# Kernel optimization log

Measured on AMD Instinct MI355X. Metric: run time of the kernel, lower is better.

Reference implementation:

```python
import jax, jax.numpy as jnp
import numpy as np

E, N, C, A, S, H, HD, RH = 320000, 20000, 128, 4, 16, 8, 32, 64
AH = H * HD  # 256 attn-head channels; mul_alpha = AH, mul_alpha_head = HD
OUT = 128


def smooth_leaky_relu(x, a=0.2):
    # Equiformer SmoothLeakyReLU: 0.5*((1+a)*x + (1-a)*x*(2*sigmoid(x)-1))
    return 0.5 * ((1 + a) * x + (1 - a) * x * (2.0 * jax.nn.sigmoid(x) - 1.0))


def setup_inputs() -> dict:
    key = jax.random.key(0)
    ks = jax.random.split(key, 20)
    d = {
        'message': jax.random.normal(ks[0], (E, C), jnp.float32),
        'edge_attr': jax.random.normal(ks[1], (E, A), jnp.float32),
        'edge_scalars': jax.random.normal(ks[2], (E, S), jnp.float32),
        'w_rad1': jax.random.normal(ks[3], (S, RH), jnp.float32) / np.sqrt(S),
        'b_rad1': jnp.zeros((RH,), jnp.float32),
        'w_rad2': jax.random.normal(ks[4], (RH, C * A), jnp.float32) / np.sqrt(RH),
        'b_rad2': jnp.zeros((C * A,), jnp.float32),
        'w_dtp_v': jax.random.normal(ks[5], (C, A), jnp.float32) / np.sqrt(A),
        'w_lin_act': jax.random.normal(ks[6], (C, C), jnp.float32) / np.sqrt(C),
        'b_lin_act': jnp.zeros((C,), jnp.float32),
        'w_alpha': jax.random.normal(ks[7], (C, AH), jnp.float32) / np.sqrt(C),
        'b_alpha': jnp.zeros((AH,), jnp.float32),
        'w_lin_v': jax.random.normal(ks[8], (C, AH), jnp.float32) / np.sqrt(C),
        'b_lin_v': jnp.zeros((AH,), jnp.float32),
        'alpha_dot': jax.random.normal(ks[9], (H, HD), jnp.float32) / np.sqrt(HD),
        'w_proj': jax.random.normal(ks[10], (AH, OUT), jnp.float32) / np.sqrt(AH),
        'b_proj': jnp.zeros((OUT,), jnp.float32),
        'edge_dst': jax.random.randint(ks[11], (E,), 0, N, jnp.int32),
        'n_nodes_dst': N,
    }
    return d


def reference(message, edge_attr, edge_scalars,
              w_rad1, b_rad1, w_rad2, b_rad2,
              w_dtp_v, w_lin_act, b_lin_act,
              w_alpha, b_alpha, w_lin_v, b_lin_v,
              alpha_dot, w_proj, b_proj,
              edge_dst, n_nodes_dst):
    n = n_nodes_dst
    # dtp_rad: radial MLP -> per-edge depthwise TP weights [E, C, A]
    h = jax.nn.silu(edge_scalars @ w_rad1 + b_rad1)
    w = (h @ w_rad2 + b_rad2).reshape(-1, C, A)
    # sep_act.dtp (scalar irreps): out[e,c] = msg[e,c] * sum_a w[e,c,a]*attr[e,a]
    msg = message * jnp.einsum('eca,ea->ec', w, edge_attr)
    # sep_alpha -> alpha heads [E, H, HD]
    alpha = (msg @ w_alpha + b_alpha).reshape(-1, H, HD)
    # sep_act.lin + gate (scalars -> SiLU)
    value = jax.nn.silu(msg @ w_lin_act + b_lin_act)
    # sep_value: internal-weight dtp then linear, reshape to heads
    value = value * jnp.einsum('ca,ea->ec', w_dtp_v, edge_attr)
    value = (value @ w_lin_v + b_lin_v).reshape(-1, H, HD)
    # attention logits
    alpha = smooth_leaky_relu(alpha)
    alpha = jnp.einsum('ehk,hk->eh', alpha, alpha_dot)
    # scatter softmax over destination nodes
    amax = jax.ops.segment_max(alpha, edge_dst, num_segments=n)  # [N, H]
    amax = jnp.where(jnp.isfinite(amax), amax, 0.0)
    ex = jnp.exp(alpha - amax[edge_dst])
    denom = jax.ops.segment_sum(ex, edge_dst, num_segments=n)
    alpha = ex / (denom[edge_dst] + 1e-16)
    # weighted scatter-add aggregation
    attn = value * alpha[..., None]  # [E, H, HD]
    node = jax.ops.segment_sum(attn, edge_dst, num_segments=n)  # [N, H, HD]
    node = node.reshape(n, AH)  # heads2vec
    return node @ w_proj + b_proj
```

## Files before the change

### kernel.cpp

```cpp
#include <hip/hip_runtime.h>
#include <hip/hip_bf16.h>

#define C_   128
#define A_   4
#define S_   16
#define RH_  64
#define H_   8
#define AH_  256
#define OUT_ 128

typedef __attribute__((ext_vector_type(8))) short bf16x8;
typedef __attribute__((ext_vector_type(4))) float f32x4;

__device__ __forceinline__ float sigf(float x) { return 1.0f / (1.0f + __expf(-x)); }

__device__ __forceinline__ unsigned short f2bf(float x) {
    unsigned u = __float_as_uint(x);
    unsigned r = (u + 0x7fffu + ((u >> 16) & 1u)) >> 16;
    return (unsigned short)r;
}
__device__ __forceinline__ float bf2f(unsigned short v) {
    return __uint_as_float((unsigned)v << 16);
}

__device__ __forceinline__ unsigned pkbf(float a, float b) {
    union { __hip_bfloat162 h; unsigned u; } c;
    c.h = __float22bfloat162_rn(float2{a, b});
    return c.u;
}

__device__ __forceinline__ unsigned enc(float x) {
    unsigned b = __float_as_uint(x);
    return (b & 0x80000000u) ? ~b : (b | 0x80000000u);
}
__device__ __forceinline__ float dec(unsigned u) {
    unsigned b = (u & 0x80000000u) ? (u & 0x7fffffffu) : ~u;
    return __uint_as_float(b);
}

__global__ void k_pack(const float* __restrict__ W, short* __restrict__ out, int K, int N) {
    const int KS = K / 32;
    const int ct = blockIdx.x / KS, ks = blockIdx.x % KS;
    const int l = threadIdx.x, lr = l & 15, lg = l >> 4;
    bf16x8 v;
    #pragma unroll
    for (int j = 0; j < 8; j++)
        v[j] = (short)f2bf(W[(size_t)(ks * 32 + lg * 8 + j) * N + ct * 16 + lr]);
    *(bf16x8*)&out[((size_t)blockIdx.x * 64 + l) * 8] = v;
}

__global__ void k_pack_dtp(const float* __restrict__ W, short* __restrict__ out) {
    const int ct = blockIdx.x >> 3, ks = blockIdx.x & 7;
    const int l = threadIdx.x, lr = l & 15, lg = l >> 4;
    bf16x8 v;
    #pragma unroll
    for (int j = 0; j < 8; j++)
        v[j] = (short)f2bf(W[(size_t)(ks * 8 + lg * 2 + (j >> 2)) * 512 + (ct * 16 + lr) * 4 + (j & 3)]);
    *(bf16x8*)&out[((size_t)blockIdx.x * 64 + l) * 8] = v;
}

__global__ __launch_bounds__(256) void k_hist(
    const int* __restrict__ edge_dst, int* __restrict__ deg, int E)
{
    const int e = blockIdx.x * 256 + threadIdx.x;
    if (e < E) atomicAdd(&deg[edge_dst[e]], 1);
}

__global__ __launch_bounds__(1024) void k_scan(
    const int* __restrict__ deg, int* __restrict__ cursor, int N)
{
    __shared__ int part[1024];
    const int t = threadIdx.x;
    const int per = (N + 1023) / 1024;
    const int i0 = t * per;
    int s = 0;
    for (int i = 0; i < per; i++) { int idx = i0 + i; if (idx < N) s += deg[idx]; }
    part[t] = s;
    __syncthreads();
    for (int off = 1; off < 1024; off <<= 1) {
        int v = (t >= off) ? part[t - off] : 0;
        __syncthreads();
        part[t] += v;
        __syncthreads();
    }
    int excl = (t == 0) ? 0 : part[t - 1];
    for (int i = 0; i < per; i++) {
        int idx = i0 + i;
        if (idx < N) { cursor[idx] = excl; excl += deg[idx]; }
    }
}

__global__ __launch_bounds__(256) void k_fill(
    const int* __restrict__ edge_dst, int* __restrict__ cursor,
    int* __restrict__ sorted, int E)
{
    const int e = blockIdx.x * 256 + threadIdx.x;
    if (e < E) {
        const int pos = atomicAdd(&cursor[edge_dst[e]], 1);
        sorted[pos] = e;
    }
}

__global__ __launch_bounds__(256, 4) void k_msgalpha(
    const float* __restrict__ message, const float* __restrict__ edge_attr,
    const float* __restrict__ edge_scalars,
    const float* __restrict__ w_rad1, const float* __restrict__ b_rad1,
    const short* __restrict__ w_rad2_lin, const float* __restrict__ b_rad2,
    const short* __restrict__ w_alpha_lin, const float* __restrict__ b_alpha,
    const float* __restrict__ alpha_dot, const int* __restrict__ edge_dst,
    short* __restrict__ msg_bf, float* __restrict__ logits, unsigned* __restrict__ amax_u)
{
    __shared__ __align__(16) char smem[25216];
    short* Ap     = (short*)smem;
    short* msg_s  = (short*)(smem + 16384);
    float* w1_s   = (float*)(smem + 16384);
    float* es_s   = (float*)(smem + 16384 + 4096);
    float* attr_s = (float*)(smem + 24576);
    int*   dst_s  = (int*)(smem + 25088);

    const int t = threadIdx.x;
    const long e0 = (long)blockIdx.x * 32;

    *(float4*)&w1_s[t * 4] = *(const float4*)&w_rad1[t * 4];
    if (t < 128) {
        const int r = t >> 2, s4 = (t & 3) * 4;
        *(float4*)&es_s[r * 17 + s4] = *(const float4*)&edge_scalars[(e0 + r) * S_ + s4];
    }
    if (t < 32) {
        *(float4*)&attr_s[t * 4] = *(const float4*)&edge_attr[(e0 + t) * A_];
        dst_s[t] = edge_dst[e0 + t];
    }
    __syncthreads();

    {
        const int r = t & 31, o0 = (t >> 5) * 8;
        float acc[8];
        #pragma unroll
        for (int i = 0; i < 8; i++) acc[i] = b_rad1[o0 + i];
        #pragma unroll
        for (int s = 0; s < S_; s++) {
            const float ev = es_s[r * 17 + s];
            #pragma unroll
            for (int i = 0; i < 8; i++) acc[i] += ev * w1_s[s * 64 + o0 + i];
        }
        float h[8];
        #pragma unroll
        for (int i = 0; i < 8; i++) { const float x = acc[i]; h[i] = x * sigf(x); }
        const float4 a4 = *(const float4*)&attr_s[r * 4];
        char* base = (char*)Ap + r * 512;
        const int sw = (r & 31) << 4;
        #pragma unroll
        for (int c = 0; c < 4; c++) {
            const float h0 = h[2 * c], h1 = h[2 * c + 1];
            uint4 v;
            v.x = pkbf(h0 * a4.x, h0 * a4.y);
            v.y = pkbf(h0 * a4.z, h0 * a4.w);
            v.z = pkbf(h1 * a4.x, h1 * a4.y);
            v.w = pkbf(h1 * a4.z, h1 * a4.w);
            *(uint4*)(base + ((o0 * 8 + c * 16) ^ sw)) = v;
        }
    }
    __syncthreads();

    const int w = t >> 6, l = t & 63, lr = l & 15, lg = l >> 4;

    {
        #pragma unroll
        for (int q = 0; q < 2; q++) {
            const int ct = w * 2 + q;
            bf16x8 bf[8];
            #pragma unroll
            for (int ks = 0; ks < 8; ks++)
                bf[ks] = *(const bf16x8*)&w_rad2_lin[((size_t)(ct * 8 + ks) * 64 + l) * 8];
            const int col = ct * 16 + lr;
            const float4 b2 = *(const float4*)&b_rad2[col * 4];
            #pragma unroll
            for (int rt = 0; rt < 2; rt++) {
                const int arow = rt * 16 + lr;
                const char* abase = (char*)Ap + arow * 512;
                const int asw = (arow & 31) << 4;
                bf16x8 af[8];
                #pragma unroll
                for (int ks = 0; ks < 8; ks++)
                    af[ks] = *(const bf16x8*)(abase + ((ks * 64 + lg * 16) ^ asw));
                f32x4 acc = {0.f, 0.f, 0.f, 0.f};
                #pragma unroll
                for (int ks = 0; ks < 8; ks++)
                    acc = __builtin_amdgcn_mfma_f32_16x16x32_bf16(af[ks], bf[ks], acc, 0, 0, 0);
                #pragma unroll
                for (int r = 0; r < 4; r++) {
                    const int row = rt * 16 + lg * 4 + r;
                    const float4 a4 = *(const float4*)&attr_s[row * 4];
                    const float badj = a4.x * b2.x + a4.y * b2.y + a4.z * b2.z + a4.w * b2.w;
                    const float m = message[(e0 + row) * C_ + col];
                    *(short*)((char*)msg_s + row * 256 + ((col * 2) ^ ((row & 15) << 4))) =
                        (short)f2bf(m * (acc[r] + badj));
                }
            }
        }
    }
    __syncthreads();

    {
        #pragma unroll
        for (int i = 0; i < 2; i++) {
            const int q = t + i * 256;
            const int row = q >> 4, ch = q & 15;
            const uint4 v = *(const uint4*)((char*)msg_s + row * 256 + ((ch * 16) ^ ((row & 15) << 4)));
            *(uint4*)((char*)msg_bf + ((e0 + row) * 256 + ch * 16)) = v;
        }
    }

    {
        #pragma unroll
        for (int hq = 0; hq < 2; hq++) {
            const int hd = w * 2 + hq;
            bf16x8 waf[2][4];
            float4 ba4[2], ad4[2];
            #pragma unroll
            for (int q = 0; q < 2; q++) {
                const int ctw = hd * 2 + q;
                #pragma unroll
                for (int ks = 0; ks < 4; ks++)
                    waf[q][ks] = *(const bf16x8*)&w_alpha_lin[((size_t)(ctw * 4 + ks) * 64 + l) * 8];
                ba4[q] = *(const float4*)&b_alpha[ctw * 16 + lg * 4];
                ad4[q] = *(const float4*)&alpha_dot[ctw * 16 + lg * 4];
            }
            #pragma unroll
            for (int ct = 0; ct < 2; ct++) {
                const int erow = ct * 16 + lr;
                const char* mbase = (char*)msg_s + erow * 256;
                const int msw = (erow & 15) << 4;
                bf16x8 mb[4];
                #pragma unroll
                for (int ks = 0; ks < 4; ks++)
                    mb[ks] = *(const bf16x8*)(mbase + ((ks * 64 + lg * 16) ^ msw));
                float s = 0.f;
                #pragma unroll
                for (int q = 0; q < 2; q++) {
                    f32x4 acc = {0.f, 0.f, 0.f, 0.f};
                    #pragma unroll
                    for (int ks = 0; ks < 4; ks++)
                        acc = __builtin_amdgcn_mfma_f32_16x16x32_bf16(waf[q][ks], mb[ks], acc, 0, 0, 0);
                    #pragma unroll
                    for (int r = 0; r < 4; r++) {
                        const float x = acc[r] + ((const float*)&ba4[q])[r];
                        const float y = x * (0.2f + 0.8f * sigf(x));
                        s += y * ((const float*)&ad4[q])[r];
                    }
                }
                s += __shfl_xor(s, 16);
                s += __shfl_xor(s, 32);
                if (lg == 0) {
                    const long e = e0 + ct * 16 + lr;
                    logits[e * H_ + hd] = s;
                    atomicMax(&amax_u[dst_s[ct * 16 + lr] * H_ + hd], enc(s));
                }
            }
        }
    }
}

__global__ __launch_bounds__(256) void k_denom(
    const float* __restrict__ logits, const int* __restrict__ edge_dst,
    const unsigned* __restrict__ amax_u, float* __restrict__ denom, int EH)
{
    const int t = blockIdx.x * 256 + threadIdx.x;
    if (t >= EH) return;
    const int e = t >> 3, h = t & 7;
    const int n = edge_dst[e];
    const float am = dec(amax_u[n * H_ + h]);
    atomicAdd(&denom[n * H_ + h], __expf(logits[t] - am));
}

__global__ __launch_bounds__(256, 5) void k_value(
    const short* __restrict__ msg_bf, const float* __restrict__ edge_attr,
    const short* __restrict__ w_lin_act_lin, const float* __restrict__ b_lin_act,
    const float* __restrict__ w_dtp_v,
    const short* __restrict__ w_lin_v_lin, const float* __restrict__ b_lin_v,
    const float* __restrict__ logits, const int* __restrict__ edge_dst,
    const unsigned* __restrict__ amax_u, const float* __restrict__ denom,
    const int* __restrict__ sorted, float* __restrict__ node)
{
    __shared__ __align__(16) char pool[16896];
    __shared__ float attr_s[32][4];
    __shared__ float wgt_s[32][H_];
    __shared__ int   dst_s[32];
    __shared__ int   eid_s[32];
    short* a_s  = (short*)pool;
    short* v_s  = (short*)(pool + 8192);
    short* val2 = (short*)pool;

    const int t = threadIdx.x;
    const int b0 = blockIdx.x * 32;

    if (t < 32) {
        const int e = sorted[b0 + t];
        eid_s[t] = e;
        dst_s[t] = edge_dst[e];
        *(float4*)&attr_s[t][0] = *(const float4*)&edge_attr[(long)e * A_];
    }
    __syncthreads();
    #pragma unroll
    for (int i = 0; i < 2; i++) {
        const int q = t + i * 256;
        const int row = q >> 4, ch = q & 15;
        const uint4 v = *(const uint4*)((const char*)msg_bf + ((long)eid_s[row] * 256 + ch * 16));
        *(uint4*)((char*)a_s + row * 256 + ((ch * 16) ^ ((row & 15) << 4))) = v;
    }
    {
        const int el = t >> 3, h = t & 7;
        const long e = eid_s[el];
        const int n = dst_s[el];
        const float am = dec(amax_u[n * H_ + h]);
        const float d  = denom[n * H_ + h];
        wgt_s[el][h] = __expf(logits[e * H_ + h] - am) / (d + 1e-16f);
    }
    __syncthreads();

    const int w = t >> 6, l = t & 63, lr = l & 15, lg = l >> 4;
    {
        bf16x8 af[2][4];
        #pragma unroll
        for (int rt = 0; rt < 2; rt++)
            #pragma unroll
            for (int ks = 0; ks < 4; ks++) {
                const int arow = rt * 16 + lr;
                af[rt][ks] = *(bf16x8*)((char*)a_s + arow * 256 + ((ks * 64 + lg * 16) ^ ((arow & 15) << 4)));
            }
        #pragma unroll
        for (int q = 0; q < 2; q++) {
            const int ct = w * 2 + q;
            bf16x8 bfg[4];
            #pragma unroll
            for (int ks = 0; ks < 4; ks++)
                bfg[ks] = *(const bf16x8*)&w_lin_act_lin[((size_t)(ct * 4 + ks) * 64 + l) * 8];
            const int col = ct * 16 + lr;
            const float bb = b_lin_act[col];
            const float4 wv = *(const float4*)&w_dtp_v[col * 4];
            #pragma unroll
            for (int rt = 0; rt < 2; rt++) {
                f32x4 acc = {0.f, 0.f, 0.f, 0.f};
                #pragma unroll
                for (int ks = 0; ks < 4; ks++)
                    acc = __builtin_amdgcn_mfma_f32_16x16x32_bf16(af[rt][ks], bfg[ks], acc, 0, 0, 0);
                #pragma unroll
                for (int r = 0; r < 4; r++) {
                    const int row = rt * 16 + lg * 4 + r;
                    float x = acc[r] + bb;
                    x = x * sigf(x);
                    const float4 a4 = *(const float4*)&attr_s[row][0];
                    const float dv = wv.x * a4.x + wv.y * a4.y + wv.z * a4.z + wv.w * a4.w;
                    *(short*)((char*)v_s + row * 256 + ((col * 2) ^ ((row & 15) << 4))) =
                        (short)f2bf(x * dv);
                }
            }
        }
    }
    __syncthreads();

    bf16x8 vf[2][4];
    #pragma unroll
    for (int rt = 0; rt < 2; rt++)
        #pragma unroll
        for (int ks = 0; ks < 4; ks++) {
            const int row = rt * 16 + lr;
            vf[rt][ks] = *(bf16x8*)((char*)v_s + row * 256 + ((ks * 64 + lg * 16) ^ ((row & 15) << 4)));
        }
    __syncthreads();

    #pragma unroll
    for (int q = 0; q < 4; q++) {
        const int ct = w * 4 + q;
        bf16x8 bf[4];
        #pragma unroll
        for (int ks = 0; ks < 4; ks++)
            bf[ks] = *(const bf16x8*)&w_lin_v_lin[((size_t)(ct * 4 + ks) * 64 + l) * 8];
        const int col = ct * 16 + lr;
        const float bb = b_lin_v[col];
        #pragma unroll
        for (int rt = 0; rt < 2; rt++) {
            f32x4 acc = {0.f, 0.f, 0.f, 0.f};
            #pragma unroll
            for (int ks = 0; ks < 4; ks++)
                acc = __builtin_amdgcn_mfma_f32_16x16x32_bf16(vf[rt][ks], bf[ks], acc, 0, 0, 0);
            #pragma unroll
            for (int r = 0; r < 4; r++) {
                const int row = rt * 16 + lg * 4 + r;
                val2[row * 264 + col] = (short)f2bf((acc[r] + bb) * wgt_s[row][col >> 5]);
            }
        }
    }
    __syncthreads();
    {
        const int c = t;
        float run = 0.f;
        int s = 0;
        #pragma unroll 1
        for (int e = 0; e < 32; e++) {
            run += bf2f((unsigned short)val2[e * 264 + c]);
            const bool end = (e == 31) || (dst_s[e + 1] != dst_s[e]);
            if (end) {
                float* np = node + (long)dst_s[e] * AH_ + c;
                if (s == 0 || e == 31) atomicAdd(np, run);
                else *np = run;
                run = 0.f; s = e + 1;
            }
        }
    }
}

__global__ __launch_bounds__(256) void k_proj(
    const float* __restrict__ node, const float* __restrict__ w_proj,
    const float* __restrict__ b_proj, float* __restrict__ out)
{
    __shared__ float node_s[32][AH_];
    const int t = threadIdx.x;
    const long n0 = (long)blockIdx.x * 32;
    #pragma unroll
    for (int i = 0; i < 8; i++) {
        const int idx = t + i * 256;
        const int nl = idx >> 6, c4 = (idx & 63) * 4;
        *(float4*)&node_s[nl][c4] = *(const float4*)&node[(n0 + nl) * AH_ + c4];
    }
    __syncthreads();
    const int j0 = (t & 31) * 4;
    const int g  = t >> 5;
    float4 acc4[4];
    const float4 b = *(const float4*)&b_proj[j0];
    #pragma unroll
    for (int i = 0; i < 4; i++) acc4[i] = b;
    const float* wp = w_proj + j0;
    for (int c4 = 0; c4 < 64; c4++) {
        const float4 w0 = *(const float4*)&wp[(c4 * 4 + 0) * OUT_];
        const float4 w1 = *(const float4*)&wp[(c4 * 4 + 1) * OUT_];
        const float4 w2 = *(const float4*)&wp[(c4 * 4 + 2) * OUT_];
        const float4 w3 = *(const float4*)&wp[(c4 * 4 + 3) * OUT_];
        #pragma unroll
        for (int i = 0; i < 4; i++) {
            const float4 nv = *(const float4*)&node_s[g * 4 + i][c4 * 4];
            acc4[i].x += nv.x * w0.x + nv.y * w1.x + nv.z * w2.x + nv.w * w3.x;
            acc4[i].y += nv.x * w0.y + nv.y * w1.y + nv.z * w2.y + nv.w * w3.y;
            acc4[i].z += nv.x * w0.z + nv.y * w1.z + nv.z * w2.z + nv.w * w3.z;
            acc4[i].w += nv.x * w0.w + nv.y * w1.w + nv.z * w2.w + nv.w * w3.w;
        }
    }
    #pragma unroll
    for (int i = 0; i < 4; i++) {
        const long n = n0 + g * 4 + i;
        *(float4*)&out[n * OUT_ + j0] = acc4[i];
    }
}

extern "C" void kernel_launch(void* const* d_in, const int* in_sizes, int n_in,
                              void* d_out, int out_size, void* d_ws, size_t ws_size,
                              hipStream_t stream)
{
    const float* message      = (const float*)d_in[0];
    const float* edge_attr    = (const float*)d_in[1];
    const float* edge_scalars = (const float*)d_in[2];
    const float* w_rad1       = (const float*)d_in[3];
    const float* b_rad1       = (const float*)d_in[4];
    const float* w_rad2       = (const float*)d_in[5];
    const float* b_rad2       = (const float*)d_in[6];
    const float* w_dtp_v      = (const float*)d_in[7];
    const float* w_lin_act    = (const float*)d_in[8];
    const float* b_lin_act    = (const float*)d_in[9];
    const float* w_alpha      = (const float*)d_in[10];
    const float* b_alpha      = (const float*)d_in[11];
    const float* w_lin_v      = (const float*)d_in[12];
    const float* b_lin_v      = (const float*)d_in[13];
    const float* alpha_dot    = (const float*)d_in[14];
    const float* w_proj       = (const float*)d_in[15];
    const float* b_proj       = (const float*)d_in[16];
    const int*   edge_dst     = (const int*)d_in[17];

    const int E = in_sizes[0] / C_;
    const int N = out_size / OUT_;

    char* ws = (char*)d_ws;
    float*    node     = (float*)ws;
    unsigned* amax_u   = (unsigned*)(node + (size_t)N * AH_);
    float*    denom    = (float*)(amax_u + (size_t)N * H_);
    int*      deg      = (int*)(denom + (size_t)N * H_);
    int*      cursor   = deg + N;
    int*      sorted   = cursor + N;
    short*    w_rad2_l = (short*)(sorted + E);
    short*    w_alph_l = w_rad2_l + 64 * 512;
    short*    w_lact_l = w_alph_l + 128 * 256;
    short*    w_linv_l = w_lact_l + 128 * 128;
    short*    msg_bf   = w_linv_l + 128 * 256;
    float*    logits   = (float*)(msg_bf + (size_t)E * C_);

    hipMemsetAsync(d_ws, 0, (size_t)N * (AH_ + 2 * H_ + 1) * 4, stream);

    const int nbE256 = (E + 255) / 256;
    k_pack_dtp<<<64, 64, 0, stream>>>(w_rad2, w_rad2_l);
    k_pack<<<(256/16)*(128/32), 64, 0, stream>>>(w_alpha,   w_alph_l, 128, 256);
    k_pack<<<(128/16)*(128/32), 64, 0, stream>>>(w_lin_act, w_lact_l, 128, 128);
    k_pack<<<(256/16)*(128/32), 64, 0, stream>>>(w_lin_v,   w_linv_l, 128, 256);
    k_hist<<<nbE256, 256, 0, stream>>>(edge_dst, deg, E);
    k_scan<<<1, 1024, 0, stream>>>(deg, cursor, N);
    k_fill<<<nbE256, 256, 0, stream>>>(edge_dst, cursor, sorted, E);
    k_msgalpha<<<E / 32, 256, 0, stream>>>(message, edge_attr, edge_scalars,
                                           w_rad1, b_rad1, w_rad2_l, b_rad2,
                                           w_alph_l, b_alpha, alpha_dot, edge_dst,
                                           msg_bf, logits, amax_u);
    k_denom<<<(E * H_ + 255) / 256, 256, 0, stream>>>(logits, edge_dst, amax_u, denom, E * H_);
    k_value<<<E / 32, 256, 0, stream>>>(msg_bf, edge_attr, w_lact_l, b_lin_act, w_dtp_v,
                                        w_linv_l, b_lin_v, logits, edge_dst, amax_u, denom,
                                        sorted, node);
    k_proj<<<N / 32, 256, 0, stream>>>(node, w_proj, b_proj, (float*)d_out);
}
```

Before: 407.2 us.

## Cut register pressure in msgalpha and aggregate softmax denominators over sorted edges

```diff
diff --git a/kernel.cpp b/kernel.cpp
--- a/kernel.cpp
+++ b/kernel.cpp
@@ -101,7 +101,7 @@
     }
 }
 
-__global__ __launch_bounds__(256, 4) void k_msgalpha(
+__global__ __launch_bounds__(256, 5) void k_msgalpha(
     const float* __restrict__ message, const float* __restrict__ edge_attr,
     const float* __restrict__ edge_scalars,
     const float* __restrict__ w_rad1, const float* __restrict__ b_rad1,
@@ -168,10 +168,6 @@
         #pragma unroll
         for (int q = 0; q < 2; q++) {
             const int ct = w * 2 + q;
-            bf16x8 bf[8];
-            #pragma unroll
-            for (int ks = 0; ks < 8; ks++)
-                bf[ks] = *(const bf16x8*)&w_rad2_lin[((size_t)(ct * 8 + ks) * 64 + l) * 8];
             const int col = ct * 16 + lr;
             const float4 b2 = *(const float4*)&b_rad2[col * 4];
             #pragma unroll
@@ -179,14 +175,19 @@
                 const int arow = rt * 16 + lr;
                 const char* abase = (char*)Ap + arow * 512;
                 const int asw = (arow & 31) << 4;
-                bf16x8 af[8];
-                #pragma unroll
-                for (int ks = 0; ks < 8; ks++)
-                    af[ks] = *(const bf16x8*)(abase + ((ks * 64 + lg * 16) ^ asw));
                 f32x4 acc = {0.f, 0.f, 0.f, 0.f};
                 #pragma unroll
-                for (int ks = 0; ks < 8; ks++)
-                    acc = __builtin_amdgcn_mfma_f32_16x16x32_bf16(af[ks], bf[ks], acc, 0, 0, 0);
+                for (int kc = 0; kc < 2; kc++) {
+                    bf16x8 bf[4], af[4];
+                    #pragma unroll
+                    for (int ks = 0; ks < 4; ks++) {
+                        bf[ks] = *(const bf16x8*)&w_rad2_lin[((size_t)(ct * 8 + kc * 4 + ks) * 64 + l) * 8];
+                        af[ks] = *(const bf16x8*)(abase + (((kc * 4 + ks) * 64 + lg * 16) ^ asw));
+                    }
+                    #pragma unroll
+                    for (int ks = 0; ks < 4; ks++)
+                        acc = __builtin_amdgcn_mfma_f32_16x16x32_bf16(af[ks], bf[ks], acc, 0, 0, 0);
+                }
                 #pragma unroll
                 for (int r = 0; r < 4; r++) {
                     const int row = rt * 16 + lg * 4 + r;
@@ -215,46 +216,46 @@
         #pragma unroll
         for (int hq = 0; hq < 2; hq++) {
             const int hd = w * 2 + hq;
-            bf16x8 waf[2][4];
-            float4 ba4[2], ad4[2];
+            float s0 = 0.f, s1 = 0.f;
             #pragma unroll
             for (int q = 0; q < 2; q++) {
                 const int ctw = hd * 2 + q;
+                bf16x8 waf[4];
                 #pragma unroll
                 for (int ks = 0; ks < 4; ks++)
-                    waf[q][ks] = *(const bf16x8*)&w_alpha_lin[((size_t)(ctw * 4 + ks) * 64 + l) * 8];
-                ba4[q] = *(const float4*)&b_alpha[ctw * 16 + lg * 4];
-                ad4[q] = *(const float4*)&alpha_dot[ctw * 16 + lg * 4];
-            }
-            #pragma unroll
-            for (int ct = 0; ct < 2; ct++) {
-                const int erow = ct * 16 + lr;
-                const char* mbase = (char*)msg_s + erow * 256;
-                const int msw = (erow & 15) << 4;
-                bf16x8 mb[4];
+                    waf[ks] = *(const bf16x8*)&w_alpha_lin[((size_t)(ctw * 4 + ks) * 64 + l) * 8];
+                const float4 ba4 = *(const float4*)&b_alpha[ctw * 16 + lg * 4];
+                const float4 ad4 = *(const float4*)&alpha_dot[ctw * 16 + lg * 4];
                 #pragma unroll
-                for (int ks = 0; ks < 4; ks++)
-                    mb[ks] = *(const bf16x8*)(mbase + ((ks * 64 + lg * 16) ^ msw));
-                float s = 0.f;
-                #pragma unroll
-                for (int q = 0; q < 2; q++) {
+                for (int ct = 0; ct < 2; ct++) {
+                    const int erow = ct * 16 + lr;
+                    const char* mbase = (char*)msg_s + erow * 256;
+                    const int msw = (erow & 15) << 4;
                     f32x4 acc = {0.f, 0.f, 0.f, 0.f};
                     #pragma unroll
-                    for (int ks = 0; ks < 4; ks++)
-                        acc = __builtin_amdgcn_mfma_f32_16x16x32_bf16(waf[q][ks], mb[ks], acc, 0, 0, 0);
+                    for (int ks = 0; ks < 4; ks++) {
+                        const bf16x8 mb = *(const bf16x8*)(mbase + ((ks * 64 + lg * 16) ^ msw));
+                        acc = __builtin_amdgcn_mfma_f32_16x16x32_bf16(waf[ks], mb, acc, 0, 0, 0);
+                    }
+                    float sl = 0.f;
                     #pragma unroll
                     for (int r = 0; r < 4; r++) {
-                        const float x = acc[r] + ((const float*)&ba4[q])[r];
+                        const float x = acc[r] + ((const float*)&ba4)[r];
                         const float y = x * (0.2f + 0.8f * sigf(x));
-                        s += y * ((const float*)&ad4[q])[r];
+                        sl += y * ((const float*)&ad4)[r];
                     }
+                    if (ct == 0) s0 += sl; else s1 += sl;
                 }
-                s += __shfl_xor(s, 16);
-                s += __shfl_xor(s, 32);
+            }
+            #pragma unroll
+            for (int ct = 0; ct < 2; ct++) {
+                float v = (ct == 0) ? s0 : s1;
+                v += __shfl_xor(v, 16);
+                v += __shfl_xor(v, 32);
                 if (lg == 0) {
                     const long e = e0 + ct * 16 + lr;
-                    logits[e * H_ + hd] = s;
-                    atomicMax(&amax_u[dst_s[ct * 16 + lr] * H_ + hd], enc(s));
+                    logits[e * H_ + hd] = v;
+                    atomicMax(&amax_u[dst_s[ct * 16 + lr] * H_ + hd], enc(v));
                 }
             }
         }
@@ -263,14 +264,25 @@
 
 __global__ __launch_bounds__(256) void k_denom(
     const float* __restrict__ logits, const int* __restrict__ edge_dst,
-    const unsigned* __restrict__ amax_u, float* __restrict__ denom, int EH)
-{
-    const int t = blockIdx.x * 256 + threadIdx.x;
-    if (t >= EH) return;
-    const int e = t >> 3, h = t & 7;
-    const int n = edge_dst[e];
-    const float am = dec(amax_u[n * H_ + h]);
-    atomicAdd(&denom[n * H_ + h], __expf(logits[t] - am));
+    const int* __restrict__ sorted, const unsigned* __restrict__ amax_u,
+    float* __restrict__ denom, int E)
+{
+    const int idx = blockIdx.x * 256 + threadIdx.x;
+    if (idx >= E) return;
+    const int g = idx >> 3, h = idx & 7;
+    int nprev = -1; float run = 0.f, am = 0.f;
+    #pragma unroll 1
+    for (int e = 0; e < 8; e++) {
+        const int eid = sorted[g * 8 + e];
+        const int n = edge_dst[eid];
+        if (n != nprev) {
+            if (nprev >= 0) atomicAdd(&denom[nprev * H_ + h], run);
+            nprev = n; run = 0.f;
+            am = dec(amax_u[n * H_ + h]);
+        }
+        run += __expf(logits[(size_t)eid * H_ + h] - am);
+    }
+    atomicAdd(&denom[nprev * H_ + h], run);
 }
 
 __global__ __launch_bounds__(256, 5) void k_value(
@@ -506,7 +518,7 @@
                                            w_rad1, b_rad1, w_rad2_l, b_rad2,
                                            w_alph_l, b_alpha, alpha_dot, edge_dst,
                                            msg_bf, logits, amax_u);
-    k_denom<<<(E * H_ + 255) / 256, 256, 0, stream>>>(logits, edge_dst, amax_u, denom, E * H_);
+    k_denom<<<nbE256, 256, 0, stream>>>(logits, edge_dst, sorted, amax_u, denom, E);
     k_value<<<E / 32, 256, 0, stream>>>(msg_bf, edge_attr, w_lact_l, b_lin_act, w_dtp_v,
                                         w_linv_l, b_lin_v, logits, edge_dst, amax_u, denom,
                                         sorted, node);
```

After: 436.8 us. 7.3% more time.
